# Kernel tuning notes

Hardware: AMD Instinct MI355X
Metric: run time of the kernel (lower is better)

The kernel has to match this reference:

```python
import jax, jax.numpy as jnp
import numpy as np

B, C, FS, Z_DIM, OUT_C, F_SIZE = 256, 512, 16, 64, 1, 3
NZ = FS * FS  # 256


def setup_inputs() -> dict:
    key = jax.random.key(0)
    k1, k2, k3, k4, k5 = jax.random.split(key, 5)
    # z: [B, C, H, W]
    z = jax.random.normal(k1, (B, C, FS, FS), dtype=jnp.float32)
    # 512 independent per-channel Linear(Nz -> z_dim): stacked weights/biases
    lim_in = 1.0 / np.sqrt(NZ)
    W_in = jax.random.uniform(k2, (C, NZ, Z_DIM), minval=-lim_in, maxval=lim_in, dtype=jnp.float32)
    b_in = jax.random.uniform(k3, (C, Z_DIM), minval=-lim_in, maxval=lim_in, dtype=jnp.float32)
    # shared Linear(z_dim -> out_channels*f_size*f_size)
    lim_out = 1.0 / np.sqrt(Z_DIM)
    W_out = jax.random.uniform(k4, (Z_DIM, OUT_C * F_SIZE * F_SIZE), minval=-lim_out, maxval=lim_out, dtype=jnp.float32)
    b_out = jax.random.uniform(k5, (OUT_C * F_SIZE * F_SIZE,), minval=-lim_out, maxval=lim_out, dtype=jnp.float32)
    return {"z": z, "W_in": W_in, "b_in": b_in, "W_out": W_out, "b_out": b_out}


def reference(z, W_in, b_in, W_out, b_out):
    batch = z.shape[0]
    # flatten each channel's HxW map: [B, C, Nz]
    x = z.reshape(batch, C, NZ)
    # per-channel Linear as one batched GEMM: [B, C, z_dim]
    a = jnp.einsum('bcn,cnz->bcz', x, W_in) + b_in[None, :, :]
    # shared output Linear: [B, C, out_c*f*f]
    k = jnp.einsum('bcz,zk->bck', a, W_out) + b_out
    # [B, C, out_channels, f_size, f_size]
    return k.reshape(batch, C, OUT_C, F_SIZE, F_SIZE)
```

## Files before the change

### kernel.cpp

```cpp
#include <hip/hip_runtime.h>

#define BB 256
#define CC 512
#define NZ 256
#define ZD 64
#define KK 9

template<int CTRL>
__device__ __forceinline__ float dpp_add(float v) {
    int o = __builtin_amdgcn_update_dpp(0, __float_as_int(v), CTRL, 0xF, 0xF, true);
    return v + __int_as_float(o);
}
__device__ __forceinline__ float red8(float v) {
    v = dpp_add<0xB1>(v);
    v = dpp_add<0x4E>(v);
    v = dpp_add<0x141>(v);
    return v;
}

__global__ __launch_bounds__(512, 2)
void wf_kernel(const float* __restrict__ W_in,
               const float* __restrict__ b_in,
               const float* __restrict__ W_out,
               const float* __restrict__ b_out,
               float* __restrict__ wf,
               float* __restrict__ bk) {
    __shared__ __align__(16) float s_woutT[KK * ZD];
    __shared__ float s_bin[ZD];

    const int c = blockIdx.x;
    const int t = threadIdx.x;

    for (int i = t; i < KK * ZD; i += 512) {
        float v = W_out[i];
        int zz = i / KK, k = i - zz * KK;
        s_woutT[k * ZD + zz] = v;
    }
    if (t < ZD) s_bin[t] = b_in[c * ZD + t];
    __syncthreads();

    const int n = t >> 1, half = t & 1;
    const float* wrow = W_in + ((size_t)c * NZ + n) * ZD + half * 32;
    float acc[KK];
#pragma unroll
    for (int k = 0; k < KK; ++k) acc[k] = 0.f;
#pragma unroll
    for (int j = 0; j < 8; ++j) {
        const float4 w = *reinterpret_cast<const float4*>(wrow + 4 * j);
#pragma unroll
        for (int k = 0; k < KK; ++k) {
            const float4 wo = *reinterpret_cast<const float4*>(
                &s_woutT[k * ZD + half * 32 + 4 * j]);
            acc[k] += w.x * wo.x + w.y * wo.y + w.z * wo.z + w.w * wo.w;
        }
    }
#pragma unroll
    for (int k = 0; k < KK; ++k) acc[k] = dpp_add<0xB1>(acc[k]);
    if (half == 0) {
#pragma unroll
        for (int k = 0; k < KK; ++k) wf[((size_t)c * KK + k) * NZ + n] = acc[k];
    }
    if (t < KK) {
        float s = 0.f;
        for (int zz = 0; zz < ZD; ++zz) s += s_bin[zz] * s_woutT[t * ZD + zz];
        bk[c * KK + t] = s + b_out[t];
    }
}

__global__ __launch_bounds__(256, 2)
void out_kernel(const float* __restrict__ z,
                const float* __restrict__ wf,
                const float* __restrict__ bk,
                float* __restrict__ out) {
    __shared__ __align__(16) float s_wfT[KK * NZ];
    __shared__ float s_biask[KK];

    const int c = blockIdx.x;
    const int bh = blockIdx.y;
    const int t = threadIdx.x;

    {
        const float4* src = reinterpret_cast<const float4*>(wf + (size_t)c * KK * NZ);
        float4* dst = reinterpret_cast<float4*>(s_wfT);
        for (int i = t; i < KK * NZ / 4; i += 256) dst[i] = src[i];
        if (t < KK) s_biask[t] = bk[c * KK + t];
    }
    __syncthreads();

    const int lane = t & 63;
    const int wave = t >> 6;
    const int g = lane >> 3;
    const int sub = lane & 7;
    const int b0 = bh * 128 + wave * 32 + g * 4;
    const float biasS = s_biask[sub];
    const float bias8 = s_biask[8];

    const float* xp = z + ((size_t)b0 * CC + c) * NZ + sub * 4;
    const size_t bstr = (size_t)CC * NZ;

    float acc[4][KK];
#pragma unroll
    for (int bb = 0; bb < 4; ++bb)
#pragma unroll
        for (int k = 0; k < KK; ++k) acc[bb][k] = 0.f;

    float4 xb[3][4];
#pragma unroll
    for (int bb = 0; bb < 4; ++bb)
        xb[0][bb] = *reinterpret_cast<const float4*>(xp + bb * bstr);
#pragma unroll
    for (int bb = 0; bb < 4; ++bb)
        xb[1][bb] = *reinterpret_cast<const float4*>(xp + bb * bstr + 32);

#pragma unroll
    for (int j = 0; j < 8; ++j) {
        if (j < 6) {
#pragma unroll
            for (int bb = 0; bb < 4; ++bb)
                xb[(j + 2) % 3][bb] =
                    *reinterpret_cast<const float4*>(xp + bb * bstr + (j + 2) * 32);
        }
#pragma unroll
        for (int k = 0; k < KK; ++k) {
            const float4 wfv = *reinterpret_cast<const float4*>(
                &s_wfT[k * NZ + sub * 4 + j * 32]);
#pragma unroll
            for (int bb = 0; bb < 4; ++bb) {
                const float4 x = xb[j % 3][bb];
                acc[bb][k] += x.x * wfv.x + x.y * wfv.y + x.z * wfv.z + x.w * wfv.w;
            }
        }
    }

#pragma unroll
    for (int bb = 0; bb < 4; ++bb)
#pragma unroll
        for (int k = 0; k < KK; ++k) acc[bb][k] = red8(acc[bb][k]);

#pragma unroll
    for (int bb = 0; bb < 4; ++bb) {
        float v = acc[bb][0];
#pragma unroll
        for (int k = 1; k < 8; ++k) {
            if (sub == k) v = acc[bb][k];
        }
        const size_t o0 = ((size_t)(b0 + bb) * CC + c) * KK;
        out[o0 + sub] = v + biasS;
        if (sub == 0) out[o0 + 8] = acc[bb][8] + bias8;
    }
}

__global__ __launch_bounds__(512, 2)
void hyper_kernel(const float* __restrict__ z,
                  const float* __restrict__ W_in,
                  const float* __restrict__ b_in,
                  const float* __restrict__ W_out,
                  const float* __restrict__ b_out,
                  float* __restrict__ out) {
    __shared__ __align__(16) float s_wfT[KK * NZ];
    __shared__ __align__(16) float s_woutT[KK * ZD];
    __shared__ float s_bin[ZD];
    __shared__ float s_biask[KK];

    const int c = blockIdx.x;
    const int t = threadIdx.x;

    for (int i = t; i < KK * ZD; i += 512) {
        float v = W_out[i];
        int zz = i / KK, k = i - zz * KK;
        s_woutT[k * ZD + zz] = v;
    }
    if (t < ZD) s_bin[t] = b_in[c * ZD + t];
    __syncthreads();

    {
        const int n = t >> 1, half = t & 1;
        const float* wrow = W_in + ((size_t)c * NZ + n) * ZD + half * 32;
        float acc[KK];
#pragma unroll
        for (int k = 0; k < KK; ++k) acc[k] = 0.f;
#pragma unroll
        for (int j = 0; j < 8; ++j) {
            const float4 w = *reinterpret_cast<const float4*>(wrow + 4 * j);
#pragma unroll
            for (int k = 0; k < KK; ++k) {
                const float4 wo = *reinterpret_cast<const float4*>(
                    &s_woutT[k * ZD + half * 32 + 4 * j]);
                acc[k] += w.x * wo.x + w.y * wo.y + w.z * wo.z + w.w * wo.w;
            }
        }
#pragma unroll
        for (int k = 0; k < KK; ++k) acc[k] = dpp_add<0xB1>(acc[k]);
        if (half == 0) {
#pragma unroll
            for (int k = 0; k < KK; ++k) s_wfT[k * NZ + n] = acc[k];
        }
        if (t < KK) {
            float s = 0.f;
            for (int zz = 0; zz < ZD; ++zz) s += s_bin[zz] * s_woutT[t * ZD + zz];
            s_biask[t] = s + b_out[t];
        }
    }
    __syncthreads();

    const int lane = t & 63;
    const int wave = t >> 6;
    const int g = lane >> 3;
    const int sub = lane & 7;
    const int b0 = wave * 32 + g * 4;
    const float biasS = s_biask[sub];
    const float bias8 = s_biask[8];

    const float* xp = z + ((size_t)b0 * CC + c) * NZ + sub * 4;
    const size_t bstr = (size_t)CC * NZ;

    float acc[4][KK];
#pragma unroll
    for (int bb = 0; bb < 4; ++bb)
#pragma unroll
        for (int k = 0; k < KK; ++k) acc[bb][k] = 0.f;

    float4 xb[2][4];
#pragma unroll
    for (int bb = 0; bb < 4; ++bb)
        xb[0][bb] = *reinterpret_cast<const float4*>(xp + bb * bstr);

#pragma unroll
    for (int j = 0; j < 8; ++j) {
        if (j < 7) {
#pragma unroll
            for (int bb = 0; bb < 4; ++bb)
                xb[(j + 1) & 1][bb] =
                    *reinterpret_cast<const float4*>(xp + bb * bstr + (j + 1) * 32);
        }
#pragma unroll
        for (int k = 0; k < KK; ++k) {
            const float4 wfv = *reinterpret_cast<const float4*>(
                &s_wfT[k * NZ + sub * 4 + j * 32]);
#pragma unroll
            for (int bb = 0; bb < 4; ++bb) {
                const float4 x = xb[j & 1][bb];
                acc[bb][k] += x.x * wfv.x + x.y * wfv.y + x.z * wfv.z + x.w * wfv.w;
            }
        }
    }

#pragma unroll
    for (int bb = 0; bb < 4; ++bb)
#pragma unroll
        for (int k = 0; k < KK; ++k) acc[bb][k] = red8(acc[bb][k]);

#pragma unroll
    for (int bb = 0; bb < 4; ++bb) {
        float v = acc[bb][0];
#pragma unroll
        for (int k = 1; k < 8; ++k) {
            if (sub == k) v = acc[bb][k];
        }
        const size_t o0 = ((size_t)(b0 + bb) * CC + c) * KK;
        out[o0 + sub] = v + biasS;
        if (sub == 0) out[o0 + 8] = acc[bb][8] + bias8;
    }
}

extern "C" void kernel_launch(void* const* d_in, const int* in_sizes, int n_in,
                              void* d_out, int out_size, void* d_ws, size_t ws_size,
                              hipStream_t stream) {
    const float* z     = (const float*)d_in[0];
    const float* W_in  = (const float*)d_in[1];
    const float* b_in  = (const float*)d_in[2];
    const float* W_out = (const float*)d_in[3];
    const float* b_out = (const float*)d_in[4];
    float* out = (float*)d_out;

    const size_t WF_ELTS = (size_t)CC * KK * NZ;
    const size_t BK_ELTS = (size_t)CC * KK;
    const size_t NEED = (WF_ELTS + BK_ELTS) * sizeof(float);

    if (d_ws != nullptr && ws_size >= NEED) {
        float* wf = (float*)d_ws;
        float* bk = wf + WF_ELTS;
        wf_kernel<<<dim3(CC), dim3(512), 0, stream>>>(W_in, b_in, W_out, b_out, wf, bk);
        out_kernel<<<dim3(CC, 2), dim3(256), 0, stream>>>(z, wf, bk, out);
    } else {
        hyper_kernel<<<dim3(CC), dim3(512), 0, stream>>>(z, W_in, b_in, W_out, b_out, out);
    }
}
```

Baseline: 232.5 us.

## Stage z rows through per-wave LDS with coalesced loads and register prefetch

```diff
diff --git a/kernel.cpp b/kernel.cpp
--- a/kernel.cpp
+++ b/kernel.cpp
@@ -74,10 +74,15 @@
                 float* __restrict__ out) {
     __shared__ __align__(16) float s_wfT[KK * NZ];
     __shared__ float s_biask[KK];
+    __shared__ __align__(16) float s_z[4][8 * NZ];
 
     const int c = blockIdx.x;
     const int bh = blockIdx.y;
     const int t = threadIdx.x;
+    const int lane = t & 63;
+    const int wave = t >> 6;
+    const int g = lane >> 3;
+    const int sub = lane & 7;
 
     {
         const float4* src = reinterpret_cast<const float4*>(wf + (size_t)c * KK * NZ);
@@ -85,68 +90,60 @@
         for (int i = t; i < KK * NZ / 4; i += 256) dst[i] = src[i];
         if (t < KK) s_biask[t] = bk[c * KK + t];
     }
-    __syncthreads();
-
-    const int lane = t & 63;
-    const int wave = t >> 6;
-    const int g = lane >> 3;
-    const int sub = lane & 7;
-    const int b0 = bh * 128 + wave * 32 + g * 4;
+
+    const size_t bstr = (size_t)CC * NZ;
+    const int base_b = bh * 128 + wave * 32;
+    const float* zw = z + ((size_t)base_b * CC + c) * NZ + lane * 4;
+
+    float4 xr[8];
+#pragma unroll
+    for (int i = 0; i < 8; ++i)
+        xr[i] = *reinterpret_cast<const float4*>(zw + (size_t)i * bstr);
+
+    __syncthreads();
+
+    float* myz = s_z[wave];
     const float biasS = s_biask[sub];
     const float bias8 = s_biask[8];
 
-    const float* xp = z + ((size_t)b0 * CC + c) * NZ + sub * 4;
-    const size_t bstr = (size_t)CC * NZ;
-
-    float acc[4][KK];
-#pragma unroll
-    for (int bb = 0; bb < 4; ++bb)
-#pragma unroll
-        for (int k = 0; k < KK; ++k) acc[bb][k] = 0.f;
-
-    float4 xb[3][4];
-#pragma unroll
-    for (int bb = 0; bb < 4; ++bb)
-        xb[0][bb] = *reinterpret_cast<const float4*>(xp + bb * bstr);
-#pragma unroll
-    for (int bb = 0; bb < 4; ++bb)
-        xb[1][bb] = *reinterpret_cast<const float4*>(xp + bb * bstr + 32);
-
-#pragma unroll
-    for (int j = 0; j < 8; ++j) {
-        if (j < 6) {
-#pragma unroll
-            for (int bb = 0; bb < 4; ++bb)
-                xb[(j + 2) % 3][bb] =
-                    *reinterpret_cast<const float4*>(xp + bb * bstr + (j + 2) * 32);
-        }
-#pragma unroll
-        for (int k = 0; k < KK; ++k) {
-            const float4 wfv = *reinterpret_cast<const float4*>(
-                &s_wfT[k * NZ + sub * 4 + j * 32]);
-#pragma unroll
-            for (int bb = 0; bb < 4; ++bb) {
-                const float4 x = xb[j % 3][bb];
-                acc[bb][k] += x.x * wfv.x + x.y * wfv.y + x.z * wfv.z + x.w * wfv.w;
+    for (int q = 0; q < 4; ++q) {
+#pragma unroll
+        for (int i = 0; i < 8; ++i)
+            *reinterpret_cast<float4*>(&myz[i * NZ + lane * 4]) = xr[i];
+
+        if (q < 3) {
+            const float* zn = zw + (size_t)(q + 1) * 8 * bstr;
+#pragma unroll
+            for (int i = 0; i < 8; ++i)
+                xr[i] = *reinterpret_cast<const float4*>(zn + (size_t)i * bstr);
+        }
+
+        float acc[KK];
+#pragma unroll
+        for (int k = 0; k < KK; ++k) acc[k] = 0.f;
+#pragma unroll
+        for (int j = 0; j < 8; ++j) {
+            const float4 x = *reinterpret_cast<const float4*>(
+                &myz[g * NZ + j * 32 + sub * 4]);
+#pragma unroll
+            for (int k = 0; k < KK; ++k) {
+                const float4 w = *reinterpret_cast<const float4*>(
+                    &s_wfT[k * NZ + j * 32 + sub * 4]);
+                acc[k] += x.x * w.x + x.y * w.y + x.z * w.z + x.w * w.w;
             }
         }
-    }
-
-#pragma unroll
-    for (int bb = 0; bb < 4; ++bb)
-#pragma unroll
-        for (int k = 0; k < KK; ++k) acc[bb][k] = red8(acc[bb][k]);
-
-#pragma unroll
-    for (int bb = 0; bb < 4; ++bb) {
-        float v = acc[bb][0];
+#pragma unroll
+        for (int k = 0; k < KK; ++k) acc[k] = red8(acc[k]);
+
+        const int b = base_b + q * 8 + g;
+        float v = acc[0];
 #pragma unroll
         for (int k = 1; k < 8; ++k) {
-            if (sub == k) v = acc[bb][k];
-        }
-        const size_t o0 = ((size_t)(b0 + bb) * CC + c) * KK;
+            if (sub == k) v = acc[k];
+        }
+        const size_t o0 = ((size_t)b * CC + c) * KK;
         out[o0 + sub] = v + biasS;
-        if (sub == 0) out[o0 + 8] = acc[bb][8] + bias8;
+        if (sub == 0) out[o0 + 8] = acc[8] + bias8;
     }
 }
 
@@ -278,10 +275,10 @@
     const size_t NEED = (WF_ELTS + BK_ELTS) * sizeof(float);
 
     if (d_ws != nullptr && ws_size >= NEED) {
-        float* wf = (float*)d_ws;
-        float* bk = wf + WF_ELTS;
-        wf_kernel<<<dim3(CC), dim3(512), 0, stream>>>(W_in, b_in, W_out, b_out, wf, bk);
-        out_kernel<<<dim3(CC, 2), dim3(256), 0, stream>>>(z, wf, bk, out);
+        float* wfp = (float*)d_ws;
+        float* bkp = wfp + WF_ELTS;
+        wf_kernel<<<dim3(CC), dim3(512), 0, stream>>>(W_in, b_in, W_out, b_out, wfp, bkp);
+        out_kernel<<<dim3(CC, 2), dim3(256), 0, stream>>>(z, wfp, bkp, out);
     } else {
         hyper_kernel<<<dim3(CC), dim3(512), 0, stream>>>(z, W_in, b_in, W_out, b_out, out);
     }
```

After: 371.2 us. 1.6x slower.
